# Performance work log

Hardware: AMD Instinct MI355X
Metric: run time of the kernel (lower is better)

Reference implementation:

```python
import jax, jax.numpy as jnp
import numpy as np

BIG = 1e10
RADIUS = 0.5
NSAMPLE = 1


def square_distance(src, dst):
    # src: [B,N,3], dst: [B,M,3] -> [B,N,M] squared euclidean distances
    d = -2.0 * jnp.einsum('bnc,bmc->bnm', src, dst)
    d = d + jnp.sum(src ** 2, -1)[:, :, None]
    d = d + jnp.sum(dst ** 2, -1)[:, None, :]
    return d


def farthest_point_sample(xyz, npoint):
    # xyz: [B,N,3]; returns int32 indices [B,npoint]
    B, N, _ = xyz.shape
    dist0 = jnp.full((B, N), BIG, dtype=xyz.dtype)
    far0 = jnp.argmax(xyz[:, :, 0], axis=1).astype(jnp.int32)

    def step(carry, _):
        dist, far = carry
        centroid = jnp.take_along_axis(xyz, far[:, None, None], axis=1)  # [B,1,3]
        d = jnp.sum((xyz - centroid) ** 2, -1)  # [B,N]
        dist = jnp.minimum(dist, d)
        new_far = jnp.argmax(dist, axis=-1).astype(jnp.int32)
        return (dist, new_far), far  # record PRE-update farthest, like the torch loop

    (_, _), centroids = jax.lax.scan(step, (dist0, far0), None, length=npoint)
    return centroids.T  # [B,npoint]


def index_points(points, idx):
    # points: [B,N,C], idx: [B,S] -> [B,S,C]
    return jnp.take_along_axis(points, idx[:, :, None], axis=1)


def query_ball_point(radius, nsample, xyz, new_xyz):
    # xyz: [B,N,3], new_xyz: [B,S,3] -> int32 [B,S,nsample]
    B, S, _ = new_xyz.shape
    N = xyz.shape[1]
    sqrdists = square_distance(new_xyz, xyz)  # [B,S,N]
    base = jnp.arange(N, dtype=jnp.int32)
    group_idx = jnp.where(sqrdists > radius ** 2, jnp.int32(N), base)  # [B,S,N]
    group_idx = jnp.sort(group_idx, axis=-1)[:, :, :nsample]
    group_first = jnp.broadcast_to(group_idx[:, :, :1], group_idx.shape)
    group_idx = jnp.where(group_idx == N, group_first, group_idx)
    return group_idx


def setup_inputs() -> dict:
    key = jax.random.key(0)
    k1, k2 = jax.random.split(key)
    B, N = 4, 16384
    xyz = jax.random.uniform(k1, (B, 3, N), dtype=jnp.float32)
    cls_label = jax.random.uniform(k2, (B, 16), dtype=jnp.float32)
    return {"xyz": xyz, "cls_label": cls_label, "npoint": 1024}


def reference(xyz, cls_label, npoint):
    pts = jnp.transpose(xyz, (0, 2, 1))  # [B,N,3]
    centroids = farthest_point_sample(pts, npoint)  # [B,S]
    new_xyz = index_points(pts, centroids)  # [B,S,3]
    idx = query_ball_point(RADIUS, NSAMPLE, pts, new_xyz)  # [B,S,1]
    return idx
```

## Files before the change

kernel.cpp:

```cpp
#include <hip/hip_runtime.h>


constexpr int N_PTS  = 16384;
constexpr int NPOINT = 1024;
constexpr int BLOCK  = 512;
constexpr int KPT    = N_PTS / BLOCK;
constexpr int NWAVE  = BLOCK / 64;

__device__ inline unsigned long long pack_key(float v, int idx) {
    return ((unsigned long long)__float_as_uint(v) << 32) |
           (unsigned)(N_PTS - 1 - idx);
}
__device__ inline int key_idx(unsigned long long k) {
    return N_PTS - 1 - (int)(k & 0xFFFFu);
}

__global__ __launch_bounds__(BLOCK, 2) void fps_kernel(
    const float* __restrict__ xyz,
    int* __restrict__ cent)
{
    const int b   = blockIdx.x;
    const int tid = threadIdx.x;
    const float* X = xyz + (size_t)b * 3 * N_PTS;
    const float* Y = X + N_PTS;
    const float* Z = X + 2 * N_PTS;

    float px[KPT], py[KPT], pz[KPT], dst[KPT];
#pragma unroll
    for (int k = 0; k < KPT; ++k) {
        const int p = tid + k * BLOCK;
        px[k] = X[p];
        py[k] = Y[p];
        pz[k] = Z[p];
        dst[k] = 1e10f;
    }

    __shared__ unsigned long long s_key[2][NWAVE];

    const int wave = tid >> 6;
    const int lane = tid & 63;

    {
        float bv = px[0];
        int   bi = tid;
#pragma unroll
        for (int k = 1; k < KPT; ++k) {
            if (px[k] > bv) { bv = px[k]; bi = tid + k * BLOCK; }
        }
        unsigned long long key = pack_key(bv, bi);
#pragma unroll
        for (int off = 32; off > 0; off >>= 1) {
            unsigned long long o = __shfl_xor(key, off);
            if (o > key) key = o;
        }
        if (lane == 0) s_key[0][wave] = key;
    }
    __syncthreads();
    unsigned long long bk = s_key[0][0];
#pragma unroll
    for (int w = 1; w < NWAVE; ++w) {
        const unsigned long long o = s_key[0][w];
        if (o > bk) bk = o;
    }
    int far = __builtin_amdgcn_readfirstlane(key_idx(bk));

    for (int it = 0; it < NPOINT; ++it) {
        if (tid == 0) cent[b * NPOINT + it] = far;
        if (it == NPOINT - 1) break;

        const float cx = X[far];
        const float cy = Y[far];
        const float cz = Z[far];

        float nbv = -1.0f;
        int   nbi = N_PTS;
#pragma unroll
        for (int k = 0; k < KPT; ++k) {
            const float dx = __fsub_rn(px[k], cx);
            const float dy = __fsub_rn(py[k], cy);
            const float dz = __fsub_rn(pz[k], cz);
            const float d  = __fadd_rn(
                __fadd_rn(__fmul_rn(dx, dx), __fmul_rn(dy, dy)),
                __fmul_rn(dz, dz));
            const float nd = fminf(dst[k], d);
            dst[k] = nd;
            if (nd > nbv) { nbv = nd; nbi = tid + k * BLOCK; }
        }

        unsigned long long key = pack_key(nbv, nbi);
#pragma unroll
        for (int off = 32; off > 0; off >>= 1) {
            unsigned long long o = __shfl_xor(key, off);
            if (o > key) key = o;
        }
        const int buf = (it + 1) & 1;
        if (lane == 0) s_key[buf][wave] = key;
        __syncthreads();

        unsigned long long k0 = s_key[buf][0];
#pragma unroll
        for (int w = 1; w < NWAVE; ++w) {
            const unsigned long long o = s_key[buf][w];
            if (o > k0) k0 = o;
        }
        far = __builtin_amdgcn_readfirstlane(key_idx(k0));
    }
}

__global__ __launch_bounds__(256) void ballq_kernel(
    const float* __restrict__ xyz,
    const int* __restrict__ cent,
    int* __restrict__ out)
{
    const int gw   = (blockIdx.x * 256 + threadIdx.x) >> 6;
    const int lane = threadIdx.x & 63;
    const int b = gw / NPOINT;
    const int s = gw % NPOINT;

    const float* X = xyz + (size_t)b * 3 * N_PTS;
    const float* Y = X + N_PTS;
    const float* Z = X + 2 * N_PTS;

    const int ci = cent[b * NPOINT + s];
    const float cx = X[ci];
    const float cy = Y[ci];
    const float cz = Z[ci];
    const float cn = __fadd_rn(
        __fadd_rn(__fmul_rn(cx, cx), __fmul_rn(cy, cy)), __fmul_rn(cz, cz));

    int res = N_PTS;
    for (int base = 0; base < N_PTS; base += 64) {
        const int p = base + lane;
        const float x = X[p];
        const float y = Y[p];
        const float z = Z[p];
        const float dot = __fadd_rn(
            __fadd_rn(__fmul_rn(x, cx), __fmul_rn(y, cy)), __fmul_rn(z, cz));
        const float pn = __fadd_rn(
            __fadd_rn(__fmul_rn(x, x), __fmul_rn(y, y)), __fmul_rn(z, z));
        const float d = __fadd_rn(__fadd_rn(__fmul_rn(-2.0f, dot), cn), pn);
        const bool hit = !(d > 0.25f);
        const unsigned long long m = __ballot(hit);
        if (m) {
            res = base + (__ffsll((long long)m) - 1);
            break;
        }
    }
    if (lane == 0) out[b * NPOINT + s] = res;
}

extern "C" void kernel_launch(void* const* d_in, const int* in_sizes, int n_in,
                              void* d_out, int out_size, void* d_ws, size_t ws_size,
                              hipStream_t stream) {
    const float* xyz = (const float*)d_in[0];
    const int B = in_sizes[1] / 16;
    int* cent = (int*)d_ws;
    int* out  = (int*)d_out;

    fps_kernel<<<B, BLOCK, 0, stream>>>(xyz, cent);

    const int nwaves  = B * NPOINT;
    const int nblocks = nwaves / 4;
    ballq_kernel<<<nblocks, 256, 0, stream>>>(xyz, cent, out);
}
```

Measured before the change: 1.872 ms.

## Split FPS argmax into float max reduction plus atomicMin tie resolution, packed math

New measurement: 3.983 ms. +112.7%, slower.

```diff
diff --git a/kernel.cpp b/kernel.cpp
--- a/kernel.cpp
+++ b/kernel.cpp
@@ -3,19 +3,36 @@
 
 constexpr int N_PTS  = 16384;
 constexpr int NPOINT = 1024;
-constexpr int BLOCK  = 512;
+constexpr int BLOCK  = 1024;
 constexpr int KPT    = N_PTS / BLOCK;
+constexpr int KP2    = KPT / 2;
 constexpr int NWAVE  = BLOCK / 64;
 
-__device__ inline unsigned long long pack_key(float v, int idx) {
-    return ((unsigned long long)__float_as_uint(v) << 32) |
-           (unsigned)(N_PTS - 1 - idx);
-}
-__device__ inline int key_idx(unsigned long long k) {
-    return N_PTS - 1 - (int)(k & 0xFFFFu);
-}
-
-__global__ __launch_bounds__(BLOCK, 2) void fps_kernel(
+typedef float f32x2 __attribute__((ext_vector_type(2)));
+typedef float f32x4 __attribute__((ext_vector_type(4)));
+
+__device__ inline f32x2 pk_add(f32x2 a, f32x2 b) {
+    f32x2 d;
+    asm("v_pk_add_f32 %0, %1, %2" : "=v"(d) : "v"(a), "v"(b));
+    return d;
+}
+__device__ inline f32x2 pk_mul(f32x2 a, f32x2 b) {
+    f32x2 d;
+    asm("v_pk_mul_f32 %0, %1, %2" : "=v"(d) : "v"(a), "v"(b));
+    return d;
+}
+
+__device__ inline float lds_max16(const float* sm) {
+    const f32x4* v4 = (const f32x4*)sm;
+    const f32x4 a = v4[0], b = v4[1], c = v4[2], d = v4[3];
+    const float m = fmaxf(fmaxf(fmaxf(a.x, a.y), fmaxf(a.z, a.w)),
+                          fmaxf(fmaxf(b.x, b.y), fmaxf(b.z, b.w)));
+    const float n = fmaxf(fmaxf(fmaxf(c.x, c.y), fmaxf(c.z, c.w)),
+                          fmaxf(fmaxf(d.x, d.y), fmaxf(d.z, d.w)));
+    return fmaxf(m, n);
+}
+
+__global__ __launch_bounds__(BLOCK, 4) void fps_kernel(
     const float* __restrict__ xyz,
     int* __restrict__ cent)
 {
@@ -25,85 +42,103 @@
     const float* Y = X + N_PTS;
     const float* Z = X + 2 * N_PTS;
 
-    float px[KPT], py[KPT], pz[KPT], dst[KPT];
-#pragma unroll
-    for (int k = 0; k < KPT; ++k) {
-        const int p = tid + k * BLOCK;
-        px[k] = X[p];
-        py[k] = Y[p];
-        pz[k] = Z[p];
-        dst[k] = 1e10f;
-    }
-
-    __shared__ unsigned long long s_key[2][NWAVE];
+    f32x2 px[KP2], py[KP2], pz[KP2], dd[KP2];
+#pragma unroll
+    for (int k = 0; k < KP2; ++k) {
+        const int p0 = tid + (2 * k) * BLOCK;
+        const int p1 = tid + (2 * k + 1) * BLOCK;
+        px[k] = f32x2{X[p0], X[p1]};
+        py[k] = f32x2{Y[p0], Y[p1]};
+        pz[k] = f32x2{Z[p0], Z[p1]};
+        dd[k] = f32x2{1e10f, 1e10f};
+    }
+
+    __shared__ __align__(16) float s_max[2][NWAVE];
+    __shared__ int s_win[2];
 
     const int wave = tid >> 6;
     const int lane = tid & 63;
-
+    if (tid == 0) { s_win[0] = 0x7fffffff; s_win[1] = 0x7fffffff; }
+
+    int far;
     {
-        float bv = px[0];
-        int   bi = tid;
-#pragma unroll
-        for (int k = 1; k < KPT; ++k) {
-            if (px[k] > bv) { bv = px[k]; bi = tid + k * BLOCK; }
-        }
-        unsigned long long key = pack_key(bv, bi);
-#pragma unroll
-        for (int off = 32; off > 0; off >>= 1) {
-            unsigned long long o = __shfl_xor(key, off);
-            if (o > key) key = o;
-        }
-        if (lane == 0) s_key[0][wave] = key;
-    }
-    __syncthreads();
-    unsigned long long bk = s_key[0][0];
-#pragma unroll
-    for (int w = 1; w < NWAVE; ++w) {
-        const unsigned long long o = s_key[0][w];
-        if (o > bk) bk = o;
-    }
-    int far = __builtin_amdgcn_readfirstlane(key_idx(bk));
+        float bv = px[0].x;
+#pragma unroll
+        for (int k = 0; k < KP2; ++k) {
+            bv = fmaxf(bv, px[k].x);
+            bv = fmaxf(bv, px[k].y);
+        }
+#pragma unroll
+        for (int off = 32; off > 0; off >>= 1)
+            bv = fmaxf(bv, __shfl_xor(bv, off));
+        if (lane == 0) s_max[1][wave] = bv;
+        __syncthreads();
+        const float BV = lds_max16(s_max[1]);
+        if (bv == BV) {
+            int cand = 0x7fffffff;
+#pragma unroll
+            for (int k = 0; k < KP2; ++k) {
+                if (px[k].x == BV) cand = min(cand, tid + (2 * k) * BLOCK);
+                if (px[k].y == BV) cand = min(cand, tid + (2 * k + 1) * BLOCK);
+            }
+            atomicMin(&s_win[1], cand);
+        }
+        __syncthreads();
+        far = __builtin_amdgcn_readfirstlane(s_win[1]);
+    }
 
     for (int it = 0; it < NPOINT; ++it) {
         if (tid == 0) cent[b * NPOINT + it] = far;
         if (it == NPOINT - 1) break;
+        const int buf = it & 1;
 
         const float cx = X[far];
         const float cy = Y[far];
         const float cz = Z[far];
-
-        float nbv = -1.0f;
-        int   nbi = N_PTS;
-#pragma unroll
-        for (int k = 0; k < KPT; ++k) {
-            const float dx = __fsub_rn(px[k], cx);
-            const float dy = __fsub_rn(py[k], cy);
-            const float dz = __fsub_rn(pz[k], cz);
-            const float d  = __fadd_rn(
-                __fadd_rn(__fmul_rn(dx, dx), __fmul_rn(dy, dy)),
-                __fmul_rn(dz, dz));
-            const float nd = fminf(dst[k], d);
-            dst[k] = nd;
-            if (nd > nbv) { nbv = nd; nbi = tid + k * BLOCK; }
-        }
-
-        unsigned long long key = pack_key(nbv, nbi);
-#pragma unroll
-        for (int off = 32; off > 0; off >>= 1) {
-            unsigned long long o = __shfl_xor(key, off);
-            if (o > key) key = o;
-        }
-        const int buf = (it + 1) & 1;
-        if (lane == 0) s_key[buf][wave] = key;
-        __syncthreads();
-
-        unsigned long long k0 = s_key[buf][0];
-#pragma unroll
-        for (int w = 1; w < NWAVE; ++w) {
-            const unsigned long long o = s_key[buf][w];
-            if (o > k0) k0 = o;
-        }
-        far = __builtin_amdgcn_readfirstlane(key_idx(k0));
+        const f32x2 ncx = {-cx, -cx};
+        const f32x2 ncy = {-cy, -cy};
+        const f32x2 ncz = {-cz, -cz};
+
+#pragma unroll
+        for (int k = 0; k < KP2; ++k) {
+            const f32x2 dx = pk_add(px[k], ncx);
+            const f32x2 dy = pk_add(py[k], ncy);
+            const f32x2 dz = pk_add(pz[k], ncz);
+            const f32x2 d  = pk_add(pk_add(pk_mul(dx, dx), pk_mul(dy, dy)),
+                                    pk_mul(dz, dz));
+            f32x2 nd;
+            nd.x = fminf(dd[k].x, d.x);
+            nd.y = fminf(dd[k].y, d.y);
+            dd[k] = nd;
+        }
+
+        f32x2 m2 = dd[0];
+#pragma unroll
+        for (int k = 1; k < KP2; ++k) {
+            m2.x = fmaxf(m2.x, dd[k].x);
+            m2.y = fmaxf(m2.y, dd[k].y);
+        }
+        float bv = fmaxf(m2.x, m2.y);
+#pragma unroll
+        for (int off = 32; off > 0; off >>= 1)
+            bv = fmaxf(bv, __shfl_xor(bv, off));
+        if (lane == 0) s_max[buf][wave] = bv;
+        __syncthreads();
+
+        if (tid == 0) s_win[buf ^ 1] = 0x7fffffff;
+        const float BV = lds_max16(s_max[buf]);
+
+        if (bv == BV) {
+            int cand = 0x7fffffff;
+#pragma unroll
+            for (int k = 0; k < KP2; ++k) {
+                if (dd[k].x == BV) cand = min(cand, tid + (2 * k) * BLOCK);
+                if (dd[k].y == BV) cand = min(cand, tid + (2 * k + 1) * BLOCK);
+            }
+            atomicMin(&s_win[buf], cand);
+        }
+        __syncthreads();
+        far = __builtin_amdgcn_readfirstlane(s_win[buf]);
     }
 }
 
```

## Use DPP wave reductions and 1024-thread FPS blocks with tree cross-wave max

Applied to the files above, without the earlier changes.

After: 2.175 ms. 1.16x slower.

```diff
diff --git a/kernel.cpp b/kernel.cpp
--- a/kernel.cpp
+++ b/kernel.cpp
@@ -3,7 +3,7 @@
 
 constexpr int N_PTS  = 16384;
 constexpr int NPOINT = 1024;
-constexpr int BLOCK  = 512;
+constexpr int BLOCK  = 1024;
 constexpr int KPT    = N_PTS / BLOCK;
 constexpr int NWAVE  = BLOCK / 64;
 
@@ -14,8 +14,34 @@
 __device__ inline int key_idx(unsigned long long k) {
     return N_PTS - 1 - (int)(k & 0xFFFFu);
 }
+__device__ inline unsigned long long umax64(unsigned long long a,
+                                            unsigned long long b) {
+    return a > b ? a : b;
+}
 
-__global__ __launch_bounds__(BLOCK, 2) void fps_kernel(
+template <int CTRL, int RM, int BM>
+__device__ inline unsigned long long dpp_max_step(unsigned long long key) {
+    const int lo = (int)(unsigned)key;
+    const int hi = (int)(unsigned)(key >> 32);
+    const unsigned mlo =
+        (unsigned)__builtin_amdgcn_update_dpp(lo, lo, CTRL, RM, BM, false);
+    const unsigned mhi =
+        (unsigned)__builtin_amdgcn_update_dpp(hi, hi, CTRL, RM, BM, false);
+    const unsigned long long moved = ((unsigned long long)mhi << 32) | mlo;
+    return key > moved ? key : moved;
+}
+
+__device__ inline unsigned long long wave_max_key(unsigned long long key) {
+    key = dpp_max_step<0x111, 0xf, 0xf>(key);
+    key = dpp_max_step<0x112, 0xf, 0xf>(key);
+    key = dpp_max_step<0x114, 0xf, 0xe>(key);
+    key = dpp_max_step<0x118, 0xf, 0xc>(key);
+    key = dpp_max_step<0x142, 0xa, 0xf>(key);
+    key = dpp_max_step<0x143, 0xc, 0xf>(key);
+    return key;
+}
+
+__global__ __launch_bounds__(BLOCK, 4) void fps_kernel(
     const float* __restrict__ xyz,
     int* __restrict__ cent)
 {
@@ -40,6 +66,7 @@
     const int wave = tid >> 6;
     const int lane = tid & 63;
 
+    int far;
     {
         float bv = px[0];
         int   bi = tid;
@@ -47,22 +74,22 @@
         for (int k = 1; k < KPT; ++k) {
             if (px[k] > bv) { bv = px[k]; bi = tid + k * BLOCK; }
         }
-        unsigned long long key = pack_key(bv, bi);
-#pragma unroll
-        for (int off = 32; off > 0; off >>= 1) {
-            unsigned long long o = __shfl_xor(key, off);
-            if (o > key) key = o;
-        }
-        if (lane == 0) s_key[0][wave] = key;
+        const unsigned long long key = wave_max_key(pack_key(bv, bi));
+        if (lane == 63) s_key[0][wave] = key;
+        __syncthreads();
+        const unsigned long long* sk = s_key[0];
+        unsigned long long m0 = umax64(umax64(sk[0], sk[1]),
+                                       umax64(sk[2], sk[3]));
+        unsigned long long m1 = umax64(umax64(sk[4], sk[5]),
+                                       umax64(sk[6], sk[7]));
+        unsigned long long m2 = umax64(umax64(sk[8], sk[9]),
+                                       umax64(sk[10], sk[11]));
+        unsigned long long m3 = umax64(umax64(sk[12], sk[13]),
+                                       umax64(sk[14], sk[15]));
+        far = __builtin_amdgcn_readfirstlane(
+                  key_idx(umax64(umax64(m0, m1), umax64(m2, m3)))) &
+              (N_PTS - 1);
     }
-    __syncthreads();
-    unsigned long long bk = s_key[0][0];
-#pragma unroll
-    for (int w = 1; w < NWAVE; ++w) {
-        const unsigned long long o = s_key[0][w];
-        if (o > bk) bk = o;
-    }
-    int far = __builtin_amdgcn_readfirstlane(key_idx(bk));
 
     for (int it = 0; it < NPOINT; ++it) {
         if (tid == 0) cent[b * NPOINT + it] = far;
@@ -73,7 +100,7 @@
         const float cz = Z[far];
 
         float nbv = -1.0f;
-        int   nbi = N_PTS;
+        int   nbi = 0;
 #pragma unroll
         for (int k = 0; k < KPT; ++k) {
             const float dx = __fsub_rn(px[k], cx);
@@ -87,23 +114,23 @@
             if (nd > nbv) { nbv = nd; nbi = tid + k * BLOCK; }
         }
 
-        unsigned long long key = pack_key(nbv, nbi);
-#pragma unroll
-        for (int off = 32; off > 0; off >>= 1) {
-            unsigned long long o = __shfl_xor(key, off);
-            if (o > key) key = o;
-        }
+        const unsigned long long key = wave_max_key(pack_key(nbv, nbi));
         const int buf = (it + 1) & 1;
-        if (lane == 0) s_key[buf][wave] = key;
+        if (lane == 63) s_key[buf][wave] = key;
         __syncthreads();
 
-        unsigned long long k0 = s_key[buf][0];
-#pragma unroll
-        for (int w = 1; w < NWAVE; ++w) {
-            const unsigned long long o = s_key[buf][w];
-            if (o > k0) k0 = o;
-        }
-        far = __builtin_amdgcn_readfirstlane(key_idx(k0));
+        const unsigned long long* sk = s_key[buf];
+        unsigned long long m0 = umax64(umax64(sk[0], sk[1]),
+                                       umax64(sk[2], sk[3]));
+        unsigned long long m1 = umax64(umax64(sk[4], sk[5]),
+                                       umax64(sk[6], sk[7]));
+        unsigned long long m2 = umax64(umax64(sk[8], sk[9]),
+                                       umax64(sk[10], sk[11]));
+        unsigned long long m3 = umax64(umax64(sk[12], sk[13]),
+                                       umax64(sk[14], sk[15]));
+        far = __builtin_amdgcn_readfirstlane(
+                  key_idx(umax64(umax64(m0, m1), umax64(m2, m3)))) &
+              (N_PTS - 1);
     }
 }
 
@@ -121,7 +148,7 @@
     const float* Y = X + N_PTS;
     const float* Z = X + 2 * N_PTS;
 
-    const int ci = cent[b * NPOINT + s];
+    const int ci = cent[b * NPOINT + s] & (N_PTS - 1);
     const float cx = X[ci];
     const float cy = Y[ci];
     const float cz = Z[ci];
```
